# Optimization experiments

Hardware: AMD Instinct MI355X
Metric: run time of the kernel (lower is better)

Reference implementation:

```python
import jax, jax.numpy as jnp
import numpy as np

B, N, ATTR, H, OUT, STEPS = 8, 4096, 16, 64, 1, 8


def setup_inputs() -> dict:
    key = jax.random.key(0)
    ks = jax.random.split(key, 12)
    attr_matrix = jax.random.normal(ks[0], (B, N, ATTR), jnp.float32)
    adj_matrix = (jax.random.uniform(ks[1], (B, N, N)) < 0.01).astype(jnp.float32)
    s = float(1.0 / np.sqrt(H))
    u = lambda k, shape: jax.random.uniform(k, shape, jnp.float32, -s, s)
    Wi = jax.random.normal(ks[2], (H, ATTR), jnp.float32) * float(np.sqrt(2.0 / ATTR))  # kaiming
    bi = jnp.zeros((H,), jnp.float32)
    Wz = u(ks[3], (H, 3 * H)); bz = u(ks[4], (H,))
    Wr = u(ks[5], (H, 3 * H)); br = u(ks[6], (H,))
    Wh = u(ks[7], (H, 3 * H)); bh = u(ks[8], (H,))
    Wo = jax.random.normal(ks[9], (OUT, H), jnp.float32) * float(np.sqrt(2.0 / (H + OUT)))  # xavier
    bo = jnp.zeros((OUT,), jnp.float32)
    return dict(attr_matrix=attr_matrix, adj_matrix=adj_matrix, Wi=Wi, bi=bi,
                Wz=Wz, bz=bz, Wr=Wr, br=br, Wh=Wh, bh=bh, Wo=Wo, bo=bo)


def reference(attr_matrix, adj_matrix, Wi, bi, Wz, bz, Wr, br, Wh, bh, Wo, bo):
    # initial node states: (B, N, H)
    h = jax.nn.relu(attr_matrix @ Wi.T + bi)
    A_in = adj_matrix
    A_out = jnp.swapaxes(adj_matrix, -1, -2)
    for _ in range(STEPS):
        a_in = jnp.einsum('bij,bjh->bih', A_in, h)
        a_out = jnp.einsum('bij,bjh->bih', A_out, h)
        inp = jnp.concatenate([a_in, a_out], axis=-1)           # (B, N, 2H)
        xs = jnp.concatenate([inp, h], axis=-1)                  # (B, N, 3H)
        z = jax.nn.sigmoid(xs @ Wz.T + bz)
        r = jax.nn.sigmoid(xs @ Wr.T + br)
        hn = jnp.tanh(jnp.concatenate([inp, r * h], axis=-1) @ Wh.T + bh)
        h = (1.0 - z) * h + z * hn
    return h @ Wo.T + bo  # (B, N, OUT)
```

## Files before the change

### kernel.cpp

```cpp
#include <hip/hip_runtime.h>
#include <hip/hip_fp16.h>
#include <stdint.h>

#define BB 8
#define NN 4096
#define ATTRD 16
#define HD 64
#define STEPS 8
#define NODES (BB*NN)
#define ECAP 96
#define KPAD 196

typedef _Float16 half8 __attribute__((ext_vector_type(8)));
typedef float floatx4 __attribute__((ext_vector_type(4)));
typedef unsigned long long ull;

__global__ void init_h_kernel(const float* __restrict__ attr, const float* __restrict__ Wi,
                              const float* __restrict__ bi, float* __restrict__ h,
                              __half* __restrict__ h16) {
    int idx = blockIdx.x * blockDim.x + threadIdx.x;
    if (idx >= (NODES + 1) * HD) return;
    if (idx >= NODES * HD) {
        h16[idx] = __float2half(0.f);
        return;
    }
    int node = idx >> 6, l = idx & 63;
    const float* a = attr + node * ATTRD;
    const float* w = Wi + l * ATTRD;
    float acc = bi[l];
#pragma unroll
    for (int k = 0; k < ATTRD; k++) acc += a[k] * w[k];
    float r = acc > 0.f ? acc : 0.f;
    h[idx] = r;
    h16[idx] = __float2half(r);
}

__global__ void wprep_kernel(const float* __restrict__ Wz, const float* __restrict__ Wr,
                             const float* __restrict__ Wh,
                             _Float16* __restrict__ wf_hi, _Float16* __restrict__ wf_lo) {
    int t = blockIdx.x * blockDim.x + threadIdx.x;
    if (t >= 3 * 4 * 6 * 64 * 8) return;
    int mat = t / 12288, rem = t % 12288;
    int tile = rem / 3072, rem2 = rem % 3072;
    int kc = rem2 / 512, rem3 = rem2 % 512;
    int lane = rem3 / 8, j = rem3 % 8;
    int k = kc * 32 + (lane >> 4) * 8 + j;
    int och = tile * 16 + (lane & 15);
    const float* W = (mat == 0) ? Wz : (mat == 1) ? Wr : Wh;
    float v = W[och * 192 + k];
    _Float16 hi = (_Float16)v;
    wf_hi[t] = hi;
    wf_lo[t] = (_Float16)(v - (float)hi);
}

__global__ __launch_bounds__(256) void count_rows_kernel(const float4* __restrict__ A4,
                                                         int* __restrict__ cnt_in,
                                                         int* __restrict__ edge_in,
                                                         int* __restrict__ cnt_out,
                                                         int* __restrict__ edge_out) {
    int wave = threadIdx.x >> 6, l = threadIdx.x & 63;
    int row = blockIdx.x * 4 + wave;
    const float4* rp = A4 + (size_t)row * 1024;
    ull mask_lt = (l == 63) ? ~0ull >> 1 : ((1ull << (l + 1)) - 1) >> 1;
    float4 v[16];
#pragma unroll
    for (int t = 0; t < 16; t++) v[t] = rp[t * 64 + l];
    int colbase = (row >> 12) << 12;
    int run = 0;
    int* erow = edge_in + row * ECAP;
#pragma unroll
    for (int t = 0; t < 16; t++) {
        ull b0 = __ballot(v[t].x != 0.f);
        ull b1 = __ballot(v[t].y != 0.f);
        ull b2 = __ballot(v[t].z != 0.f);
        ull b3 = __ballot(v[t].w != 0.f);
        int pre = __popcll(b0 & mask_lt) + __popcll(b1 & mask_lt) +
                  __popcll(b2 & mask_lt) + __popcll(b3 & mask_lt);
        float vv[4] = {v[t].x, v[t].y, v[t].z, v[t].w};
        int jbase = (t * 64 + l) * 4;
        int inner = 0;
#pragma unroll
        for (int q = 0; q < 4; q++) {
            if (vv[q] != 0.f) {
                int col = colbase | (jbase + q);
                int slot = run + pre + inner;
                if (slot < ECAP) erow[slot] = col;
                inner++;
                int s2 = atomicAdd(&cnt_out[col], 1);
                if (s2 < ECAP) edge_out[col * ECAP + s2] = row;
            }
        }
        run += __popcll(b0) + __popcll(b1) + __popcll(b2) + __popcll(b3);
    }
    if (l == 0) cnt_in[row] = run;
}

__global__ __launch_bounds__(256) void aggregate_kernel(
        const uint4* __restrict__ h4, const float* __restrict__ h,
        const int* __restrict__ cnt_in, const int* __restrict__ edge_in,
        const int* __restrict__ cnt_out, const int* __restrict__ edge_out,
        float* __restrict__ xs) {
    int bid = blockIdx.x;
    int batch = bid & 7;
    int group = bid >> 3;
    int wave = threadIdx.x >> 6;
    int node = (batch << 12) + group * 4 + wave;
    int l = threadIdx.x & 63;
    int sub = l >> 3;
    int part = l & 7;
    int ni = cnt_in[node];  if (ni > ECAP) ni = ECAP;
    int no = cnt_out[node]; if (no > ECAP) no = ECAP;
    const int* ei = edge_in + node * ECAP;
    const int* eo = edge_out + node * ECAP;
    int ei0 = ei[l], ei1 = ei[64 + (l & 31)];
    int eo0 = eo[l], eo1 = eo[64 + (l & 31)];
    float ai0 = 0.f, ai1 = 0.f, ai2 = 0.f, ai3 = 0.f, ai4 = 0.f, ai5 = 0.f, ai6 = 0.f, ai7 = 0.f;
    float ao0 = 0.f, ao1 = 0.f, ao2 = 0.f, ao3 = 0.f, ao4 = 0.f, ao5 = 0.f, ao6 = 0.f, ao7 = 0.f;
    int nmax = ni > no ? ni : no;
    for (int s = 0; s < nmax; s += 8) {
        int il = s + sub;
        int gi = (il < 64) ? __shfl(ei0, il) : __shfl(ei1, il - 64);
        int go = (il < 64) ? __shfl(eo0, il) : __shfl(eo1, il - 64);
        gi = (il < ni) ? gi : NODES;
        go = (il < no) ? go : NODES;
        uint4 gA = h4[(gi << 3) | part];
        uint4 gB = h4[(go << 3) | part];
        float2 pA0 = __half22float2(*(__half2*)&gA.x);
        float2 pA1 = __half22float2(*(__half2*)&gA.y);
        float2 pA2 = __half22float2(*(__half2*)&gA.z);
        float2 pA3 = __half22float2(*(__half2*)&gA.w);
        ai0 += pA0.x; ai1 += pA0.y; ai2 += pA1.x; ai3 += pA1.y;
        ai4 += pA2.x; ai5 += pA2.y; ai6 += pA3.x; ai7 += pA3.y;
        float2 pB0 = __half22float2(*(__half2*)&gB.x);
        float2 pB1 = __half22float2(*(__half2*)&gB.y);
        float2 pB2 = __half22float2(*(__half2*)&gB.z);
        float2 pB3 = __half22float2(*(__half2*)&gB.w);
        ao0 += pB0.x; ao1 += pB0.y; ao2 += pB1.x; ao3 += pB1.y;
        ao4 += pB2.x; ao5 += pB2.y; ao6 += pB3.x; ao7 += pB3.y;
    }
#pragma unroll
    for (int off = 8; off < 64; off <<= 1) {
        ai0 += __shfl_xor(ai0, off); ai1 += __shfl_xor(ai1, off);
        ai2 += __shfl_xor(ai2, off); ai3 += __shfl_xor(ai3, off);
        ai4 += __shfl_xor(ai4, off); ai5 += __shfl_xor(ai5, off);
        ai6 += __shfl_xor(ai6, off); ai7 += __shfl_xor(ai7, off);
        ao0 += __shfl_xor(ao0, off); ao1 += __shfl_xor(ao1, off);
        ao2 += __shfl_xor(ao2, off); ao3 += __shfl_xor(ao3, off);
        ao4 += __shfl_xor(ao4, off); ao5 += __shfl_xor(ao5, off);
        ao6 += __shfl_xor(ao6, off); ao7 += __shfl_xor(ao7, off);
    }
    if (l < 8) {
        float* dst = xs + node * 192;
        float4 si0 = {ai0, ai1, ai2, ai3};
        float4 si1 = {ai4, ai5, ai6, ai7};
        float4 so0 = {ao0, ao1, ao2, ao3};
        float4 so1 = {ao4, ao5, ao6, ao7};
        *(float4*)(dst + l * 8)          = si0;
        *(float4*)(dst + l * 8 + 4)      = si1;
        *(float4*)(dst + 64 + l * 8)     = so0;
        *(float4*)(dst + 64 + l * 8 + 4) = so1;
    }
    xs[node * 192 + 128 + l] = h[(node << 6) | l];
}

__global__ __launch_bounds__(256) void gate_kernel(
        const float* __restrict__ xs_g,
        const _Float16* __restrict__ wf_hi, const _Float16* __restrict__ wf_lo,
        const float* __restrict__ bz, const float* __restrict__ br,
        const float* __restrict__ bh,
        float* __restrict__ h, __half* __restrict__ h16) {
    __shared__ float xs_t[16][KPAD];
    int bid = blockIdx.x;
    int base = ((bid & 7) << 12) | ((bid >> 3) << 4);
    int tid = threadIdx.x;
    {
        const float4* src = (const float4*)(xs_g + base * 192);
#pragma unroll
        for (int i = 0; i < 3; i++) {
            int idx = tid + i * 256;
            float4 v = src[idx];
            int nl = idx / 48, kb = (idx % 48) * 4;
            *(float4*)&xs_t[nl][kb] = v;
        }
    }
    __syncthreads();
    int wave = tid >> 6, lane = tid & 63;
    int m = lane & 15, q = lane >> 4;
    int ch = wave * 16 + m;
    const half8* WH = (const half8*)wf_hi;
    const half8* WL = (const half8*)wf_lo;

    floatx4 accz = {0.f, 0.f, 0.f, 0.f};
    floatx4 accr = {0.f, 0.f, 0.f, 0.f};
#pragma unroll
    for (int kc = 0; kc < 6; kc++) {
        const float* xr = &xs_t[m][kc * 32 + q * 8];
        float4 xa = *(const float4*)xr;
        float4 xb = *(const float4*)(xr + 4);
        float xv[8] = {xa.x, xa.y, xa.z, xa.w, xb.x, xb.y, xb.z, xb.w};
        half8 ahi, alo;
#pragma unroll
        for (int j = 0; j < 8; j++) {
            _Float16 hj = (_Float16)xv[j];
            ahi[j] = hj;
            alo[j] = (_Float16)(xv[j] - (float)hj);
        }
        half8 bzh = WH[((0 * 4 + wave) * 6 + kc) * 64 + lane];
        half8 bzl = WL[((0 * 4 + wave) * 6 + kc) * 64 + lane];
        half8 brh = WH[((1 * 4 + wave) * 6 + kc) * 64 + lane];
        half8 brl = WL[((1 * 4 + wave) * 6 + kc) * 64 + lane];
        accz = __builtin_amdgcn_mfma_f32_16x16x32_f16(ahi, bzh, accz, 0, 0, 0);
        accz = __builtin_amdgcn_mfma_f32_16x16x32_f16(alo, bzh, accz, 0, 0, 0);
        accz = __builtin_amdgcn_mfma_f32_16x16x32_f16(ahi, bzl, accz, 0, 0, 0);
        accr = __builtin_amdgcn_mfma_f32_16x16x32_f16(ahi, brh, accr, 0, 0, 0);
        accr = __builtin_amdgcn_mfma_f32_16x16x32_f16(alo, brh, accr, 0, 0, 0);
        accr = __builtin_amdgcn_mfma_f32_16x16x32_f16(ahi, brl, accr, 0, 0, 0);
    }
    float bzv = bz[ch], brv = br[ch], bhv = bh[ch];
    float zreg[4], hvreg[4], rh[4];
#pragma unroll
    for (int rg = 0; rg < 4; rg++) {
        int nl = q * 4 + rg;
        float z = 1.f / (1.f + __expf(-(accz[rg] + bzv)));
        float r = 1.f / (1.f + __expf(-(accr[rg] + brv)));
        float hv = xs_t[nl][128 + ch];
        zreg[rg] = z; hvreg[rg] = hv; rh[rg] = r * hv;
    }
    __syncthreads();
#pragma unroll
    for (int rg = 0; rg < 4; rg++) xs_t[q * 4 + rg][128 + ch] = rh[rg];
    __syncthreads();

    floatx4 acch = {0.f, 0.f, 0.f, 0.f};
#pragma unroll
    for (int kc = 0; kc < 6; kc++) {
        const float* xr = &xs_t[m][kc * 32 + q * 8];
        float4 xa = *(const float4*)xr;
        float4 xb = *(const float4*)(xr + 4);
        float xv[8] = {xa.x, xa.y, xa.z, xa.w, xb.x, xb.y, xb.z, xb.w};
        half8 ahi, alo;
#pragma unroll
        for (int j = 0; j < 8; j++) {
            _Float16 hj = (_Float16)xv[j];
            ahi[j] = hj;
            alo[j] = (_Float16)(xv[j] - (float)hj);
        }
        half8 bhh = WH[((2 * 4 + wave) * 6 + kc) * 64 + lane];
        half8 bhl = WL[((2 * 4 + wave) * 6 + kc) * 64 + lane];
        acch = __builtin_amdgcn_mfma_f32_16x16x32_f16(ahi, bhh, acch, 0, 0, 0);
        acch = __builtin_amdgcn_mfma_f32_16x16x32_f16(alo, bhh, acch, 0, 0, 0);
        acch = __builtin_amdgcn_mfma_f32_16x16x32_f16(ahi, bhl, acch, 0, 0, 0);
    }
    __syncthreads();
#pragma unroll
    for (int rg = 0; rg < 4; rg++) {
        int nl = q * 4 + rg;
        float pre = acch[rg] + bhv;
        float th = 2.f / (1.f + __expf(-2.f * pre)) - 1.f;
        float hv = hvreg[rg];
        xs_t[nl][ch] = hv + zreg[rg] * (th - hv);
    }
    __syncthreads();
    {
        int f = tid * 4;
        int nl = f >> 6, c = f & 63;
        float4 v = *(const float4*)&xs_t[nl][c];
        int gi = ((base + nl) << 6) | c;
        *(float4*)&h[gi] = v;
        __half2 p0 = {__float2half(v.x), __float2half(v.y)};
        __half2 p1 = {__float2half(v.z), __float2half(v.w)};
        *(__half2*)&h16[gi] = p0;
        *(__half2*)&h16[gi + 2] = p1;
    }
}

__global__ void out_kernel(const float* __restrict__ h, const float* __restrict__ Wo,
                           const float* __restrict__ bo, float* __restrict__ out) {
    int wid = (blockIdx.x * blockDim.x + threadIdx.x) >> 6;
    int l = threadIdx.x & 63;
    if (wid >= NODES) return;
    float p = h[(wid << 6) | l] * Wo[l];
#pragma unroll
    for (int off = 32; off > 0; off >>= 1) p += __shfl_down(p, off);
    if (l == 0) out[wid] = p + bo[0];
}

extern "C" void kernel_launch(void* const* d_in, const int* in_sizes, int n_in,
                              void* d_out, int out_size, void* d_ws, size_t ws_size,
                              hipStream_t stream) {
    const float* attr = (const float*)d_in[0];
    const float* adj  = (const float*)d_in[1];
    const float* Wi   = (const float*)d_in[2];
    const float* bi   = (const float*)d_in[3];
    const float* Wz   = (const float*)d_in[4];
    const float* bz   = (const float*)d_in[5];
    const float* Wr   = (const float*)d_in[6];
    const float* br   = (const float*)d_in[7];
    const float* Wh   = (const float*)d_in[8];
    const float* bh   = (const float*)d_in[9];
    const float* Wo   = (const float*)d_in[10];
    const float* bo   = (const float*)d_in[11];
    float* out = (float*)d_out;

    char* ws = (char*)d_ws;
    size_t off = 0;
    auto carve = [&](size_t bytes) { void* p = ws + off; off = (off + bytes + 255) & ~(size_t)255; return p; };
    float* h      = (float*)carve((size_t)NODES * HD * 4);
    __half* h16   = (__half*)carve((size_t)(NODES + 1) * HD * 2);
    float* xs     = (float*)carve((size_t)NODES * 192 * 4);
    _Float16* wf_hi = (_Float16*)carve(3 * 4 * 6 * 64 * 8 * 2);
    _Float16* wf_lo = (_Float16*)carve(3 * 4 * 6 * 64 * 8 * 2);
    int* cnt_in   = (int*)carve((size_t)NODES * 4);
    int* cnt_out  = (int*)carve((size_t)NODES * 4);
    int* edge_in  = (int*)carve((size_t)NODES * ECAP * 4);
    int* edge_out = (int*)carve((size_t)NODES * ECAP * 4);

    hipMemsetAsync(cnt_out, 0, (size_t)NODES * 4, stream);

    init_h_kernel<<<((NODES + 1) * HD + 255) / 256, 256, 0, stream>>>(attr, Wi, bi, h, h16);
    wprep_kernel<<<(3 * 4 * 6 * 64 * 8 + 255) / 256, 256, 0, stream>>>(Wz, Wr, Wh, wf_hi, wf_lo);
    count_rows_kernel<<<NODES / 4, 256, 0, stream>>>((const float4*)adj, cnt_in, edge_in,
                                                     cnt_out, edge_out);

    for (int step = 0; step < STEPS; ++step) {
        aggregate_kernel<<<NODES / 4, 256, 0, stream>>>(
            (const uint4*)h16, h, cnt_in, edge_in, cnt_out, edge_out, xs);
        gate_kernel<<<NODES / 16, 256, 0, stream>>>(xs, wf_hi, wf_lo, bz, br, bh, h, h16);
    }
    out_kernel<<<NODES * HD / 256, 256, 0, stream>>>(h, Wo, bo, out);
}
```

Baseline: 1.182 ms.

## Replace sparse edge-list gather with dense bitmask MFMA aggregation fused into GRU step

Replaces the capped edge-list construction and per-node gather aggregation with bitmasks of the adjacency (row and transposed). The bits are expanded to fp16 0/1 operands so neighbour sums become dense MFMA matmuls against a transposed fp16 copy of h staged in swizzled shared memory. Aggregation and the GRU gate computation are fused into one per-step kernel on 64-node tiles, which removes the xs round trip through global memory and halves the launches per step. In exchange it does dense work over all 4096 columns per batch, ignoring the ~1% sparsity, and uses ping-pong transposed h buffers. It also drops the ECAP truncation, so nodes with high degree are now summed in full.

```diff
diff --git a/kernel.cpp b/kernel.cpp
--- a/kernel.cpp
+++ b/kernel.cpp
@@ -8,31 +8,63 @@
 #define HD 64
 #define STEPS 8
 #define NODES (BB*NN)
-#define ECAP 96
 #define KPAD 196
+#define CHUNK 256
+#define NCHUNK (NN/CHUNK)
 
 typedef _Float16 half8 __attribute__((ext_vector_type(8)));
 typedef float floatx4 __attribute__((ext_vector_type(4)));
 typedef unsigned long long ull;
-
-__global__ void init_h_kernel(const float* __restrict__ attr, const float* __restrict__ Wi,
-                              const float* __restrict__ bi, float* __restrict__ h,
-                              __half* __restrict__ h16) {
-    int idx = blockIdx.x * blockDim.x + threadIdx.x;
-    if (idx >= (NODES + 1) * HD) return;
-    if (idx >= NODES * HD) {
-        h16[idx] = __float2half(0.f);
-        return;
-    }
-    int node = idx >> 6, l = idx & 63;
-    const float* a = attr + node * ATTRD;
-    const float* w = Wi + l * ATTRD;
-    float acc = bi[l];
-#pragma unroll
-    for (int k = 0; k < ATTRD; k++) acc += a[k] * w[k];
-    float r = acc > 0.f ? acc : 0.f;
-    h[idx] = r;
-    h16[idx] = __float2half(r);
+typedef unsigned int u32;
+
+__device__ __forceinline__ half8 expand01(u32 b) {
+    union { u32 u[4]; half8 h; } r;
+    r.u[0] = ((b & 1u)   ? 0x3C00u : 0u) | ((b & 2u)   ? 0x3C000000u : 0u);
+    r.u[1] = ((b & 4u)   ? 0x3C00u : 0u) | ((b & 8u)   ? 0x3C000000u : 0u);
+    r.u[2] = ((b & 16u)  ? 0x3C00u : 0u) | ((b & 32u)  ? 0x3C000000u : 0u);
+    r.u[3] = ((b & 64u)  ? 0x3C00u : 0u) | ((b & 128u) ? 0x3C000000u : 0u);
+    return r.h;
+}
+
+__global__ __launch_bounds__(256) void init_h_kernel(const float* __restrict__ attr,
+                                                     const float* __restrict__ Wi,
+                                                     const float* __restrict__ bi,
+                                                     float* __restrict__ h,
+                                                     _Float16* __restrict__ h16T) {
+    __shared__ float hl[64][65];
+    int bid = blockIdx.x, tid = threadIdx.x;
+    int nodeg0 = bid * 64;
+    int nl = tid >> 2, cq = tid & 3;
+    const float* a = attr + (size_t)(nodeg0 + nl) * ATTRD;
+#pragma unroll
+    for (int cc = 0; cc < 16; cc++) {
+        int c = cq * 16 + cc;
+        const float* w = Wi + c * ATTRD;
+        float acc = bi[c];
+#pragma unroll
+        for (int k = 0; k < ATTRD; k++) acc += a[k] * w[k];
+        hl[nl][c] = acc > 0.f ? acc : 0.f;
+    }
+    __syncthreads();
+#pragma unroll
+    for (int i = 0; i < 16; i++) {
+        int idx = tid + i * 256;
+        h[(size_t)nodeg0 * 64 + idx] = hl[idx >> 6][idx & 63];
+    }
+    {
+        int ch = tid & 63, seg = tid >> 6;
+        int batch = nodeg0 >> 12;
+        int nloc = (nodeg0 & 4095) + seg * 16;
+        union { ushort us[16]; uint4 u4[2]; } pk;
+#pragma unroll
+        for (int k = 0; k < 16; k++) {
+            __half hv = __float2half(hl[seg * 16 + k][ch]);
+            pk.us[k] = *(ushort*)&hv;
+        }
+        uint4* dst = (uint4*)(h16T + (size_t)batch * 64 * NN + (size_t)ch * NN + nloc);
+        dst[0] = pk.u4[0];
+        dst[1] = pk.u4[1];
+    }
 }
 
 __global__ void wprep_kernel(const float* __restrict__ Wz, const float* __restrict__ Wr,
@@ -53,148 +85,129 @@
     wf_lo[t] = (_Float16)(v - (float)hi);
 }
 
-__global__ __launch_bounds__(256) void count_rows_kernel(const float4* __restrict__ A4,
-                                                         int* __restrict__ cnt_in,
-                                                         int* __restrict__ edge_in,
-                                                         int* __restrict__ cnt_out,
-                                                         int* __restrict__ edge_out) {
+__global__ __launch_bounds__(256) void adj_bitmask_kernel(const float4* __restrict__ A4,
+                                                          ull* __restrict__ bm,
+                                                          ull* __restrict__ bmT) {
+    __shared__ unsigned char nibs[4][16][64];
     int wave = threadIdx.x >> 6, l = threadIdx.x & 63;
     int row = blockIdx.x * 4 + wave;
+    int rowl = row & 4095;
+    int colbase = row & ~4095;
     const float4* rp = A4 + (size_t)row * 1024;
-    ull mask_lt = (l == 63) ? ~0ull >> 1 : ((1ull << (l + 1)) - 1) >> 1;
     float4 v[16];
 #pragma unroll
     for (int t = 0; t < 16; t++) v[t] = rp[t * 64 + l];
-    int colbase = (row >> 12) << 12;
-    int run = 0;
-    int* erow = edge_in + row * ECAP;
 #pragma unroll
     for (int t = 0; t < 16; t++) {
-        ull b0 = __ballot(v[t].x != 0.f);
-        ull b1 = __ballot(v[t].y != 0.f);
-        ull b2 = __ballot(v[t].z != 0.f);
-        ull b3 = __ballot(v[t].w != 0.f);
-        int pre = __popcll(b0 & mask_lt) + __popcll(b1 & mask_lt) +
-                  __popcll(b2 & mask_lt) + __popcll(b3 & mask_lt);
-        float vv[4] = {v[t].x, v[t].y, v[t].z, v[t].w};
-        int jbase = (t * 64 + l) * 4;
-        int inner = 0;
-#pragma unroll
-        for (int q = 0; q < 4; q++) {
-            if (vv[q] != 0.f) {
-                int col = colbase | (jbase + q);
-                int slot = run + pre + inner;
-                if (slot < ECAP) erow[slot] = col;
-                inner++;
-                int s2 = atomicAdd(&cnt_out[col], 1);
-                if (s2 < ECAP) edge_out[col * ECAP + s2] = row;
+        float4 vv = v[t];
+        unsigned nib = (vv.x != 0.f ? 1u : 0u) | (vv.y != 0.f ? 2u : 0u) |
+                       (vv.z != 0.f ? 4u : 0u) | (vv.w != 0.f ? 8u : 0u);
+        nibs[wave][t][l] = (unsigned char)nib;
+        if (nib) {
+            int cb = 4 * (t * 64 + l);
+            float q0 = vv.x, q1 = vv.y, q2 = vv.z, q3 = vv.w;
+            ull bit = 1ull << (rowl & 63);
+            int wofs = rowl >> 6;
+            if (q0 != 0.f) atomicOr(&bmT[(size_t)(colbase + cb + 0) * 64 + wofs], bit);
+            if (q1 != 0.f) atomicOr(&bmT[(size_t)(colbase + cb + 1) * 64 + wofs], bit);
+            if (q2 != 0.f) atomicOr(&bmT[(size_t)(colbase + cb + 2) * 64 + wofs], bit);
+            if (q3 != 0.f) atomicOr(&bmT[(size_t)(colbase + cb + 3) * 64 + wofs], bit);
+        }
+    }
+    __syncthreads();
+    int r = threadIdx.x >> 6, W = threadIdx.x & 63;
+    int t = W >> 2, sub = W & 3;
+    ull wd = 0;
+#pragma unroll
+    for (int k = 0; k < 16; k++)
+        wd |= (ull)nibs[r][t][sub * 16 + k] << (4 * k);
+    bm[(size_t)(blockIdx.x * 4 + r) * 64 + W] = wd;
+}
+
+__global__ __launch_bounds__(256) void step_kernel(
+        const _Float16* __restrict__ hTin, const ull* __restrict__ bm, const ull* __restrict__ bmT,
+        const _Float16* __restrict__ wf_hi, const _Float16* __restrict__ wf_lo,
+        const float* __restrict__ bz, const float* __restrict__ br, const float* __restrict__ bh,
+        float* __restrict__ h, _Float16* __restrict__ hTout) {
+    __shared__ __attribute__((aligned(16))) float xs[64][KPAD];
+    char* smem = (char*)&xs[0][0];
+    int bid = blockIdx.x;
+    int batch = bid >> 6, tile = bid & 63;
+    int tid = threadIdx.x;
+    int w = tid >> 6, l = tid & 63;
+    int rl = l & 15, kg = l >> 4;
+    int nb = tile * 64;
+    const _Float16* hin = hTin + (size_t)batch * 64 * NN;
+    int growbase = batch * 4096 + nb + w * 16 + rl;
+    const uint2* bmrow  = (const uint2*)(bm  + (size_t)growbase * 64);
+    const uint2* bmTrow = (const uint2*)(bmT + (size_t)growbase * 64);
+
+    floatx4 accI[4], accO[4];
+#pragma unroll
+    for (int ct = 0; ct < 4; ct++) { accI[ct] = {0.f,0.f,0.f,0.f}; accO[ct] = {0.f,0.f,0.f,0.f}; }
+
+    for (int c = 0; c < NCHUNK; ++c) {
+        if (c) __syncthreads();
+        {
+            int ch = tid >> 2, part = tid & 3;
+            const uint4* gsrc = (const uint4*)(hin + (size_t)ch * NN + c * CHUNK + part * 64);
+#pragma unroll
+            for (int u = 0; u < 8; u++) {
+                uint4 d = gsrc[u];
+                int s = part * 64 + u * 8;
+                int bo = (ch * (CHUNK * 2) + s * 2) ^ ((ch & 7) << 4);
+                *(uint4*)(smem + bo) = d;
             }
         }
-        run += __popcll(b0) + __popcll(b1) + __popcll(b2) + __popcll(b3);
-    }
-    if (l == 0) cnt_in[row] = run;
-}
-
-__global__ __launch_bounds__(256) void aggregate_kernel(
-        const uint4* __restrict__ h4, const float* __restrict__ h,
-        const int* __restrict__ cnt_in, const int* __restrict__ edge_in,
-        const int* __restrict__ cnt_out, const int* __restrict__ edge_out,
-        float* __restrict__ xs) {
-    int bid = blockIdx.x;
-    int batch = bid & 7;
-    int group = bid >> 3;
-    int wave = threadIdx.x >> 6;
-    int node = (batch << 12) + group * 4 + wave;
-    int l = threadIdx.x & 63;
-    int sub = l >> 3;
-    int part = l & 7;
-    int ni = cnt_in[node];  if (ni > ECAP) ni = ECAP;
-    int no = cnt_out[node]; if (no > ECAP) no = ECAP;
-    const int* ei = edge_in + node * ECAP;
-    const int* eo = edge_out + node * ECAP;
-    int ei0 = ei[l], ei1 = ei[64 + (l & 31)];
-    int eo0 = eo[l], eo1 = eo[64 + (l & 31)];
-    float ai0 = 0.f, ai1 = 0.f, ai2 = 0.f, ai3 = 0.f, ai4 = 0.f, ai5 = 0.f, ai6 = 0.f, ai7 = 0.f;
-    float ao0 = 0.f, ao1 = 0.f, ao2 = 0.f, ao3 = 0.f, ao4 = 0.f, ao5 = 0.f, ao6 = 0.f, ao7 = 0.f;
-    int nmax = ni > no ? ni : no;
-    for (int s = 0; s < nmax; s += 8) {
-        int il = s + sub;
-        int gi = (il < 64) ? __shfl(ei0, il) : __shfl(ei1, il - 64);
-        int go = (il < 64) ? __shfl(eo0, il) : __shfl(eo1, il - 64);
-        gi = (il < ni) ? gi : NODES;
-        go = (il < no) ? go : NODES;
-        uint4 gA = h4[(gi << 3) | part];
-        uint4 gB = h4[(go << 3) | part];
-        float2 pA0 = __half22float2(*(__half2*)&gA.x);
-        float2 pA1 = __half22float2(*(__half2*)&gA.y);
-        float2 pA2 = __half22float2(*(__half2*)&gA.z);
-        float2 pA3 = __half22float2(*(__half2*)&gA.w);
-        ai0 += pA0.x; ai1 += pA0.y; ai2 += pA1.x; ai3 += pA1.y;
-        ai4 += pA2.x; ai5 += pA2.y; ai6 += pA3.x; ai7 += pA3.y;
-        float2 pB0 = __half22float2(*(__half2*)&gB.x);
-        float2 pB1 = __half22float2(*(__half2*)&gB.y);
-        float2 pB2 = __half22float2(*(__half2*)&gB.z);
-        float2 pB3 = __half22float2(*(__half2*)&gB.w);
-        ao0 += pB0.x; ao1 += pB0.y; ao2 += pB1.x; ao3 += pB1.y;
-        ao4 += pB2.x; ao5 += pB2.y; ao6 += pB3.x; ao7 += pB3.y;
-    }
-#pragma unroll
-    for (int off = 8; off < 64; off <<= 1) {
-        ai0 += __shfl_xor(ai0, off); ai1 += __shfl_xor(ai1, off);
-        ai2 += __shfl_xor(ai2, off); ai3 += __shfl_xor(ai3, off);
-        ai4 += __shfl_xor(ai4, off); ai5 += __shfl_xor(ai5, off);
-        ai6 += __shfl_xor(ai6, off); ai7 += __shfl_xor(ai7, off);
-        ao0 += __shfl_xor(ao0, off); ao1 += __shfl_xor(ao1, off);
-        ao2 += __shfl_xor(ao2, off); ao3 += __shfl_xor(ao3, off);
-        ao4 += __shfl_xor(ao4, off); ao5 += __shfl_xor(ao5, off);
-        ao6 += __shfl_xor(ao6, off); ao7 += __shfl_xor(ao7, off);
-    }
-    if (l < 8) {
-        float* dst = xs + node * 192;
-        float4 si0 = {ai0, ai1, ai2, ai3};
-        float4 si1 = {ai4, ai5, ai6, ai7};
-        float4 so0 = {ao0, ao1, ao2, ao3};
-        float4 so1 = {ao4, ao5, ao6, ao7};
-        *(float4*)(dst + l * 8)          = si0;
-        *(float4*)(dst + l * 8 + 4)      = si1;
-        *(float4*)(dst + 64 + l * 8)     = so0;
-        *(float4*)(dst + 64 + l * 8 + 4) = so1;
-    }
-    xs[node * 192 + 128 + l] = h[(node << 6) | l];
-}
-
-__global__ __launch_bounds__(256) void gate_kernel(
-        const float* __restrict__ xs_g,
-        const _Float16* __restrict__ wf_hi, const _Float16* __restrict__ wf_lo,
-        const float* __restrict__ bz, const float* __restrict__ br,
-        const float* __restrict__ bh,
-        float* __restrict__ h, __half* __restrict__ h16) {
-    __shared__ float xs_t[16][KPAD];
-    int bid = blockIdx.x;
-    int base = ((bid & 7) << 12) | ((bid >> 3) << 4);
-    int tid = threadIdx.x;
+        __syncthreads();
+        uint2 wA = bmrow[c * 4 + kg];
+        uint2 wB = bmTrow[c * 4 + kg];
+#pragma unroll
+        for (int kc = 0; kc < 8; ++kc) {
+            u32 sA = (kc & 1) ? wA.y : wA.x;
+            u32 sB = (kc & 1) ? wB.y : wB.x;
+            int srcl = rl + ((kc >> 1) << 4);
+            u32 bA = ((u32)__shfl((int)sA, srcl) >> (kg * 8)) & 255u;
+            u32 bB = ((u32)__shfl((int)sB, srcl) >> (kg * 8)) & 255u;
+            half8 aI = expand01(bA);
+            half8 aO = expand01(bB);
+#pragma unroll
+            for (int ct = 0; ct < 4; ++ct) {
+                int ch = ct * 16 + rl;
+                int bo = (ch * (CHUNK * 2) + (kc * 32 + kg * 8) * 2) ^ ((ch & 7) << 4);
+                half8 bf = *(const half8*)(smem + bo);
+                accI[ct] = __builtin_amdgcn_mfma_f32_16x16x32_f16(aI, bf, accI[ct], 0, 0, 0);
+                accO[ct] = __builtin_amdgcn_mfma_f32_16x16x32_f16(aO, bf, accO[ct], 0, 0, 0);
+            }
+        }
+    }
+    __syncthreads();
+
+#pragma unroll
+    for (int ct = 0; ct < 4; ++ct)
+#pragma unroll
+        for (int rg = 0; rg < 4; ++rg) {
+            int rowi = w * 16 + kg * 4 + rg;
+            xs[rowi][ct * 16 + rl]      = accI[ct][rg];
+            xs[rowi][64 + ct * 16 + rl] = accO[ct][rg];
+        }
     {
-        const float4* src = (const float4*)(xs_g + base * 192);
-#pragma unroll
-        for (int i = 0; i < 3; i++) {
-            int idx = tid + i * 256;
-            float4 v = src[idx];
-            int nl = idx / 48, kb = (idx % 48) * 4;
-            *(float4*)&xs_t[nl][kb] = v;
-        }
-    }
-    __syncthreads();
-    int wave = tid >> 6, lane = tid & 63;
-    int m = lane & 15, q = lane >> 4;
-    int ch = wave * 16 + m;
+        int gnode0 = batch * 4096 + nb + w * 16;
+#pragma unroll
+        for (int r = 0; r < 16; r++)
+            xs[w * 16 + r][128 + l] = h[(size_t)(gnode0 + r) * 64 + l];
+    }
+
     const half8* WH = (const half8*)wf_hi;
     const half8* WL = (const half8*)wf_lo;
-
-    floatx4 accz = {0.f, 0.f, 0.f, 0.f};
-    floatx4 accr = {0.f, 0.f, 0.f, 0.f};
+    int m = rl, q = kg;
+    int r0 = w * 16;
+    floatx4 accz[4], accr[4];
+#pragma unroll
+    for (int ct = 0; ct < 4; ct++) { accz[ct] = {0.f,0.f,0.f,0.f}; accr[ct] = {0.f,0.f,0.f,0.f}; }
 #pragma unroll
     for (int kc = 0; kc < 6; kc++) {
-        const float* xr = &xs_t[m][kc * 32 + q * 8];
+        const float* xr = &xs[r0 + m][kc * 32 + q * 8];
         float4 xa = *(const float4*)xr;
         float4 xb = *(const float4*)(xr + 4);
         float xv[8] = {xa.x, xa.y, xa.z, xa.w, xb.x, xb.y, xb.z, xb.w};
@@ -205,36 +218,39 @@
             ahi[j] = hj;
             alo[j] = (_Float16)(xv[j] - (float)hj);
         }
-        half8 bzh = WH[((0 * 4 + wave) * 6 + kc) * 64 + lane];
-        half8 bzl = WL[((0 * 4 + wave) * 6 + kc) * 64 + lane];
-        half8 brh = WH[((1 * 4 + wave) * 6 + kc) * 64 + lane];
-        half8 brl = WL[((1 * 4 + wave) * 6 + kc) * 64 + lane];
-        accz = __builtin_amdgcn_mfma_f32_16x16x32_f16(ahi, bzh, accz, 0, 0, 0);
-        accz = __builtin_amdgcn_mfma_f32_16x16x32_f16(alo, bzh, accz, 0, 0, 0);
-        accz = __builtin_amdgcn_mfma_f32_16x16x32_f16(ahi, bzl, accz, 0, 0, 0);
-        accr = __builtin_amdgcn_mfma_f32_16x16x32_f16(ahi, brh, accr, 0, 0, 0);
-        accr = __builtin_amdgcn_mfma_f32_16x16x32_f16(alo, brh, accr, 0, 0, 0);
-        accr = __builtin_amdgcn_mfma_f32_16x16x32_f16(ahi, brl, accr, 0, 0, 0);
-    }
-    float bzv = bz[ch], brv = br[ch], bhv = bh[ch];
-    float zreg[4], hvreg[4], rh[4];
-#pragma unroll
-    for (int rg = 0; rg < 4; rg++) {
-        int nl = q * 4 + rg;
-        float z = 1.f / (1.f + __expf(-(accz[rg] + bzv)));
-        float r = 1.f / (1.f + __expf(-(accr[rg] + brv)));
-        float hv = xs_t[nl][128 + ch];
-        zreg[rg] = z; hvreg[rg] = hv; rh[rg] = r * hv;
-    }
-    __syncthreads();
-#pragma unroll
-    for (int rg = 0; rg < 4; rg++) xs_t[q * 4 + rg][128 + ch] = rh[rg];
-    __syncthreads();
-
-    floatx4 acch = {0.f, 0.f, 0.f, 0.f};
+#pragma unroll
+        for (int ct = 0; ct < 4; ct++) {
+            half8 bzh = WH[((0 * 4 + ct) * 6 + kc) * 64 + l];
+            half8 bzl = WL[((0 * 4 + ct) * 6 + kc) * 64 + l];
+            half8 brh = WH[((1 * 4 + ct) * 6 + kc) * 64 + l];
+            half8 brl = WL[((1 * 4 + ct) * 6 + kc) * 64 + l];
+            accz[ct] = __builtin_amdgcn_mfma_f32_16x16x32_f16(ahi, bzh, accz[ct], 0, 0, 0);
+            accz[ct] = __builtin_amdgcn_mfma_f32_16x16x32_f16(alo, bzh, accz[ct], 0, 0, 0);
+            accz[ct] = __builtin_amdgcn_mfma_f32_16x16x32_f16(ahi, bzl, accz[ct], 0, 0, 0);
+            accr[ct] = __builtin_amdgcn_mfma_f32_16x16x32_f16(ahi, brh, accr[ct], 0, 0, 0);
+            accr[ct] = __builtin_amdgcn_mfma_f32_16x16x32_f16(alo, brh, accr[ct], 0, 0, 0);
+            accr[ct] = __builtin_amdgcn_mfma_f32_16x16x32_f16(ahi, brl, accr[ct], 0, 0, 0);
+        }
+    }
+    float zreg[4][4], hvreg[4][4];
+#pragma unroll
+    for (int ct = 0; ct < 4; ct++) {
+        float bzv = bz[ct * 16 + rl], brv = br[ct * 16 + rl];
+#pragma unroll
+        for (int rg = 0; rg < 4; rg++) {
+            float z  = 1.f / (1.f + __expf(-(accz[ct][rg] + bzv)));
+            float rr = 1.f / (1.f + __expf(-(accr[ct][rg] + brv)));
+            float hv = xs[r0 + q * 4 + rg][128 + ct * 16 + rl];
+            zreg[ct][rg] = z; hvreg[ct][rg] = hv;
+            xs[r0 + q * 4 + rg][128 + ct * 16 + rl] = rr * hv;
+        }
+    }
+    floatx4 acch[4];
+#pragma unroll
+    for (int ct = 0; ct < 4; ct++) acch[ct] = {0.f,0.f,0.f,0.f};
 #pragma unroll
     for (int kc = 0; kc < 6; kc++) {
-        const float* xr = &xs_t[m][kc * 32 + q * 8];
+        const float* xr = &xs[r0 + m][kc * 32 + q * 8];
         float4 xa = *(const float4*)xr;
         float4 xb = *(const float4*)(xr + 4);
         float xv[8] = {xa.x, xa.y, xa.z, xa.w, xb.x, xb.y, xb.z, xb.w};
@@ -245,32 +261,44 @@
             ahi[j] = hj;
             alo[j] = (_Float16)(xv[j] - (float)hj);
         }
-        half8 bhh = WH[((2 * 4 + wave) * 6 + kc) * 64 + lane];
-        half8 bhl = WL[((2 * 4 + wave) * 6 + kc) * 64 + lane];
-        acch = __builtin_amdgcn_mfma_f32_16x16x32_f16(ahi, bhh, acch, 0, 0, 0);
-        acch = __builtin_amdgcn_mfma_f32_16x16x32_f16(alo, bhh, acch, 0, 0, 0);
-        acch = __builtin_amdgcn_mfma_f32_16x16x32_f16(ahi, bhl, acch, 0, 0, 0);
-    }
-    __syncthreads();
-#pragma unroll
-    for (int rg = 0; rg < 4; rg++) {
-        int nl = q * 4 + rg;
-        float pre = acch[rg] + bhv;
-        float th = 2.f / (1.f + __expf(-2.f * pre)) - 1.f;
-        float hv = hvreg[rg];
-        xs_t[nl][ch] = hv + zreg[rg] * (th - hv);
+#pragma unroll
+        for (int ct = 0; ct < 4; ct++) {
+            half8 bhh = WH[((2 * 4 + ct) * 6 + kc) * 64 + l];
+            half8 bhl = WL[((2 * 4 + ct) * 6 + kc) * 64 + l];
+            acch[ct] = __builtin_amdgcn_mfma_f32_16x16x32_f16(ahi, bhh, acch[ct], 0, 0, 0);
+            acch[ct] = __builtin_amdgcn_mfma_f32_16x16x32_f16(alo, bhh, acch[ct], 0, 0, 0);
+            acch[ct] = __builtin_amdgcn_mfma_f32_16x16x32_f16(ahi, bhl, acch[ct], 0, 0, 0);
+        }
+    }
+#pragma unroll
+    for (int ct = 0; ct < 4; ct++) {
+        float bhv = bh[ct * 16 + rl];
+#pragma unroll
+        for (int rg = 0; rg < 4; rg++) {
+            float pre = acch[ct][rg] + bhv;
+            float th = 2.f / (1.f + __expf(-2.f * pre)) - 1.f;
+            float hv = hvreg[ct][rg];
+            xs[r0 + q * 4 + rg][ct * 16 + rl] = hv + zreg[ct][rg] * (th - hv);
+        }
+    }
+    {
+        int gnode0 = batch * 4096 + nb + w * 16;
+#pragma unroll
+        for (int r = 0; r < 16; r++)
+            h[(size_t)(gnode0 + r) * 64 + l] = xs[r0 + r][l];
     }
     __syncthreads();
     {
-        int f = tid * 4;
-        int nl = f >> 6, c = f & 63;
-        float4 v = *(const float4*)&xs_t[nl][c];
-        int gi = ((base + nl) << 6) | c;
-        *(float4*)&h[gi] = v;
-        __half2 p0 = {__float2half(v.x), __float2half(v.y)};
-        __half2 p1 = {__float2half(v.z), __float2half(v.w)};
-        *(__half2*)&h16[gi] = p0;
-        *(__half2*)&h16[gi + 2] = p1;
+        int ch = tid & 63, seg = tid >> 6;
+        union { ushort us[16]; uint4 u4[2]; } pk;
+#pragma unroll
+        for (int k = 0; k < 16; k++) {
+            __half hv = __float2half(xs[seg * 16 + k][ch]);
+            pk.us[k] = *(ushort*)&hv;
+        }
+        uint4* dst = (uint4*)(hTout + (size_t)batch * 64 * NN + (size_t)ch * NN + nb + seg * 16);
+        dst[0] = pk.u4[0];
+        dst[1] = pk.u4[1];
     }
 }
 
@@ -305,27 +333,25 @@
     char* ws = (char*)d_ws;
     size_t off = 0;
     auto carve = [&](size_t bytes) { void* p = ws + off; off = (off + bytes + 255) & ~(size_t)255; return p; };
-    float* h      = (float*)carve((size_t)NODES * HD * 4);
-    __half* h16   = (__half*)carve((size_t)(NODES + 1) * HD * 2);
-    float* xs     = (float*)carve((size_t)NODES * 192 * 4);
+    float* h        = (float*)carve((size_t)NODES * HD * 4);
+    _Float16* hTa   = (_Float16*)carve((size_t)NODES * HD * 2);
+    _Float16* hTb   = (_Float16*)carve((size_t)NODES * HD * 2);
     _Float16* wf_hi = (_Float16*)carve(3 * 4 * 6 * 64 * 8 * 2);
     _Float16* wf_lo = (_Float16*)carve(3 * 4 * 6 * 64 * 8 * 2);
-    int* cnt_in   = (int*)carve((size_t)NODES * 4);
-    int* cnt_out  = (int*)carve((size_t)NODES * 4);
-    int* edge_in  = (int*)carve((size_t)NODES * ECAP * 4);
-    int* edge_out = (int*)carve((size_t)NODES * ECAP * 4);
-
-    hipMemsetAsync(cnt_out, 0, (size_t)NODES * 4, stream);
-
-    init_h_kernel<<<((NODES + 1) * HD + 255) / 256, 256, 0, stream>>>(attr, Wi, bi, h, h16);
+    ull* bm         = (ull*)carve((size_t)NODES * 64 * 8);
+    ull* bmT        = (ull*)carve((size_t)NODES * 64 * 8);
+
+    hipMemsetAsync(bmT, 0, (size_t)NODES * 64 * 8, stream);
+
+    init_h_kernel<<<NODES / 64, 256, 0, stream>>>(attr, Wi, bi, h, hTa);
     wprep_kernel<<<(3 * 4 * 6 * 64 * 8 + 255) / 256, 256, 0, stream>>>(Wz, Wr, Wh, wf_hi, wf_lo);
-    count_rows_kernel<<<NODES / 4, 256, 0, stream>>>((const float4*)adj, cnt_in, edge_in,
-                                                     cnt_out, edge_out);
+    adj_bitmask_kernel<<<NODES / 4, 256, 0, stream>>>((const float4*)adj, bm, bmT);
 
     for (int step = 0; step < STEPS; ++step) {
-        aggregate_kernel<<<NODES / 4, 256, 0, stream>>>(
-            (const uint4*)h16, h, cnt_in, edge_in, cnt_out, edge_out, xs);
-        gate_kernel<<<NODES / 16, 256, 0, stream>>>(xs, wf_hi, wf_lo, bz, br, bh, h, h16);
+        const _Float16* hin = (step & 1) ? hTb : hTa;
+        _Float16* hout      = (step & 1) ? hTa : hTb;
+        step_kernel<<<NODES / 64, 256, 0, stream>>>(
+            hin, bm, bmT, wf_hi, wf_lo, bz, br, bh, h, hout);
     }
     out_kernel<<<NODES * HD / 256, 256, 0, stream>>>(h, Wo, bo, out);
 }
```

After: 1.463 ms. 1.24x slower.
